# Kernel tuning notes

Hardware: AMD Instinct MI355X
Metric: run time of the kernel (lower is better)

The kernel has to match this reference:

```python
import jax, jax.numpy as jnp
import numpy as np
import math

C = 16
K = 16
M = 64
DEPTH = 4          # int(sqrt(K)) tree depth
D = C * 9          # input feature dim, 9 dims per codebook subspace
N = 1024 * 128     # rows
N_NODES = K - 1    # 15 internal nodes of a depth-4 binary tree


def _selection_matrix(C):
    # node i at tree level l reads the per-codebook hashed feature at depth index l
    S = np.zeros((C * N_NODES, C * DEPTH), np.float32)
    for c in range(C):
        for i in range(N_NODES):
            level = 0 if i == 0 else (1 if i < 3 else (2 if i < 7 else 3))
            S[c * N_NODES + i, c * DEPTH + level] = 1.0
    return S


def _bit_matrix(C, K):
    # row (c,k): +/-1 on the 4 tree nodes along code k's root-to-leaf path;
    # matching code scores DEPTH, every other code scores <= DEPTH-2
    B = np.zeros((C * K, C * N_NODES), np.float32)
    for c in range(C):
        for k in range(K):
            prefix = 0
            for l in range(DEPTH):
                bit = (k >> (DEPTH - 1 - l)) & 1
                node = (2 ** l - 1) + prefix
                B[c * K + k, c * N_NODES + node] = 1.0 if bit else -1.0
                prefix = prefix * 2 + bit
    return B


def setup_inputs() -> dict:
    key = jax.random.key(0)
    k1, k2, k3, k4 = jax.random.split(key, 4)
    I = jax.random.normal(k1, (N, D), jnp.float32) - 0.5
    A = jax.random.normal(k2, (C, D // C, DEPTH), jnp.float32)   # soft hashing projections
    T = jax.random.normal(k3, (C * N_NODES,), jnp.float32)       # node thresholds
    bound = math.sqrt(1.0 / (C * K))  # kaiming_uniform with a=sqrt(5), fan_in=C*K
    L = jax.random.uniform(k4, (M, C, K), jnp.float32, -bound, bound)  # lookup tables
    S = jnp.asarray(_selection_matrix(C))
    B = jnp.asarray(_bit_matrix(C, K))
    return {"I": I, "A": A, "T": T, "L": L, "S": S, "B": B}


def reference(I, A, T, L, S, B):
    n = I.shape[0]
    # per-codebook soft hash: (n, C, D//C) x (C, D//C, DEPTH) -> (n, C*DEPTH)
    h = jnp.einsum('ncd,cdp->ncp', I.reshape(n, C, D // C), A).reshape(n, C * DEPTH)
    # thresholded tree decisions with straight-through sign
    b = h @ S.T - T                                   # (n, C*15)
    t = jnp.tanh(b)
    s = jax.lax.stop_gradient(jnp.sign(b) - t) + t    # fwd: sign, bwd: tanh'
    # bit-matrix decode of path agreements -> per-code scores
    scores = (s @ B.T).reshape(n, C, K)               # (n, C, K), max DEPTH at true code
    onehot = jax.nn.one_hot(jnp.argmax(scores, axis=2), K, dtype=I.dtype)
    E = jax.lax.stop_gradient(onehot - scores) + scores  # STE one-hot encoding
    # LUT gather-accumulate: out[n,m] = sum_c L[m,c,code(n,c)]
    return jnp.einsum('nck,mck->nm', E, L)
```

## Files before the change

kernel.cpp:

```cpp
#include <hip/hip_runtime.h>
#include <hip/hip_fp16.h>


#define NROWS (1024 * 128)

__global__ __launch_bounds__(256, 4) void halut_fwd(
    const float* __restrict__ I,
    const float* __restrict__ A,
    const float* __restrict__ T,
    const float* __restrict__ L,
    float* __restrict__ out)
{
    __shared__ uint32_t sBuf[8192];
    __shared__ double   sA[576];
    __shared__ double   sT[240];

    const int tid = threadIdx.x;

    {
        uint2* lut2 = (uint2*)sBuf;
        #pragma unroll
        for (int q = 0; q < 16; ++q) {
            const float a = L[(4 * q + 0) * 256 + tid];
            const float b = L[(4 * q + 1) * 256 + tid];
            const float c = L[(4 * q + 2) * 256 + tid];
            const float d = L[(4 * q + 3) * 256 + tid];
            uint2 u;
            u.x = ((uint32_t)__half_as_ushort(__float2half_rn(b)) << 16)
                |  (uint32_t)__half_as_ushort(__float2half_rn(a));
            u.y = ((uint32_t)__half_as_ushort(__float2half_rn(d)) << 16)
                |  (uint32_t)__half_as_ushort(__float2half_rn(c));
            lut2[q * 256 + tid] = u;
        }
    }
    for (int i = tid; i < 576; i += 256) sA[i] = (double)A[i];
    if (tid < 240) sT[tid] = (double)T[tid];
    __syncthreads();

    const int lr  = tid >> 1;
    const int mh  = tid & 1;
    const int row = blockIdx.x * 128 + lr;
    const float* rp = I + (size_t)row * 144 + mh * 72;

    float4 buf[18];
    {
        const float4* rv = (const float4*)rp;
        #pragma unroll
        for (int i = 0; i < 18; ++i) buf[i] = rv[i];
    }
    const float* bf = (const float*)buf;

    uint32_t mycodes = 0;
    #pragma unroll
    for (int cl = 0; cl < 8; ++cl) {
        const int c = mh * 8 + cl;
        double h0 = 0.0, h1 = 0.0, h2 = 0.0, h3 = 0.0;
        #pragma unroll
        for (int d = 0; d < 9; ++d) {
            const double  x  = (double)bf[cl * 9 + d];
            const double* ap = &sA[(c * 9 + d) * 4];
            h0 = fma(x, ap[0], h0);
            h1 = fma(x, ap[1], h1);
            h2 = fma(x, ap[2], h2);
            h3 = fma(x, ap[3], h3);
        }
        const double* tp = &sT[c * 15];
        int p;
        p =         (h0 > tp[0]);
        p = 2 * p + (h1 > tp[1 + p]);
        p = 2 * p + (h2 > tp[3 + p]);
        p = 2 * p + (h3 > tp[7 + p]);
        mycodes |= (uint32_t)p << (4 * cl);
    }
    const uint32_t other = __shfl_xor(mycodes, 1);
    const uint32_t lo = mh ? other : mycodes;
    const uint32_t hi = mh ? mycodes : other;

    __half2 acc2[16];
    const __half2 zero = __floats2half2_rn(0.f, 0.f);
    #pragma unroll
    for (int k = 0; k < 16; ++k) acc2[k] = zero;

    const uint2* lut2 = (const uint2*)sBuf;
    #pragma unroll 4
    for (int c = 0; c < 16; ++c) {
        const int p   = (int)(((c < 8 ? lo : hi) >> (4 * (c & 7))) & 15u);
        const int col = (c << 4) + p;
        #pragma unroll
        for (int i = 0; i < 8; ++i) {
            const uint2 w = lut2[((mh * 8 + i) << 8) + col];
            const __half2 w0 = *(const __half2*)&w.x;
            const __half2 w1 = *(const __half2*)&w.y;
            acc2[2 * i]     = __hadd2(acc2[2 * i],     w0);
            acc2[2 * i + 1] = __hadd2(acc2[2 * i + 1], w1);
        }
    }

    __syncthreads();
    float* sO = (float*)sBuf;
    #pragma unroll
    for (int k2 = 0; k2 < 8; ++k2) {
        const int ch = mh * 8 + k2;
        const float4 v = make_float4(__low2float(acc2[2 * k2]),
                                     __high2float(acc2[2 * k2]),
                                     __low2float(acc2[2 * k2 + 1]),
                                     __high2float(acc2[2 * k2 + 1]));
        *(float4*)&sO[(lr << 6) + ((ch ^ (lr & 15)) << 2)] = v;
    }
    __syncthreads();

    float4* op = (float4*)(out + (size_t)blockIdx.x * (128 * 64));
    #pragma unroll
    for (int j = 0; j < 8; ++j) {
        const int F  = tid + (j << 8);
        const int r2 = F >> 4;
        const int m2 = F & 15;
        op[F] = *(const float4*)&sO[(r2 << 6) + ((m2 ^ (r2 & 15)) << 2)];
    }
}

extern "C" void kernel_launch(void* const* d_in, const int* in_sizes, int n_in,
                              void* d_out, int out_size, void* d_ws, size_t ws_size,
                              hipStream_t stream) {
    const float* I = (const float*)d_in[0];
    const float* A = (const float*)d_in[1];
    const float* T = (const float*)d_in[2];
    const float* L = (const float*)d_in[3];
    float* outp = (float*)d_out;

    const int nblocks = NROWS / 128;
    halut_fwd<<<nblocks, 256, 0, stream>>>(I, A, T, L, outp);
}
```

Measured before the change: 31.39 us.

## Split fused kernel into code-computation and LUT-gather kernels via workspace

Splits the single fused kernel into two launches: one computes the per-row 4-bit codes from the input projections and writes them to a workspace buffer, and the other loads the LUT into shared memory and does the gather-accumulate and output store. The code kernel also loads the input row in two halves of 9 float4 instead of 18, which lowers register pressure. The intent is to shrink each kernel's register and LDS footprint so occupancy rises and memory streaming overlaps better. In exchange it adds a second launch, a global round trip for the codes, and each gather block still rebuilds the LUT in shared memory.

```diff
diff --git a/kernel.cpp b/kernel.cpp
--- a/kernel.cpp
+++ b/kernel.cpp
@@ -4,16 +4,66 @@
 
 #define NROWS (1024 * 128)
 
-__global__ __launch_bounds__(256, 4) void halut_fwd(
+__global__ __launch_bounds__(256, 4) void halut_codes(
     const float* __restrict__ I,
     const float* __restrict__ A,
     const float* __restrict__ T,
+    uint32_t* __restrict__ codes)
+{
+    __shared__ double sA[576];
+    __shared__ double sT[240];
+
+    const int tid = threadIdx.x;
+    for (int i = tid; i < 576; i += 256) sA[i] = (double)A[i];
+    if (tid < 240) sT[tid] = (double)T[tid];
+    __syncthreads();
+
+    const int lr  = tid >> 1;
+    const int mh  = tid & 1;
+    const int row = blockIdx.x * 128 + lr;
+    const float* rp = I + (size_t)row * 144 + mh * 72;
+
+    uint32_t mycodes = 0;
+    #pragma unroll
+    for (int g = 0; g < 2; ++g) {
+        float4 buf[9];
+        const float4* rv = (const float4*)(rp + g * 36);
+        #pragma unroll
+        for (int i = 0; i < 9; ++i) buf[i] = rv[i];
+        const float* bf = (const float*)buf;
+
+        #pragma unroll
+        for (int cc = 0; cc < 4; ++cc) {
+            const int cl = g * 4 + cc;
+            const int c  = mh * 8 + cl;
+            double h0 = 0.0, h1 = 0.0, h2 = 0.0, h3 = 0.0;
+            #pragma unroll
+            for (int d = 0; d < 9; ++d) {
+                const double  x  = (double)bf[cc * 9 + d];
+                const double* ap = &sA[(c * 9 + d) * 4];
+                h0 = fma(x, ap[0], h0);
+                h1 = fma(x, ap[1], h1);
+                h2 = fma(x, ap[2], h2);
+                h3 = fma(x, ap[3], h3);
+            }
+            const double* tp = &sT[c * 15];
+            int p;
+            p =         (h0 > tp[0]);
+            p = 2 * p + (h1 > tp[1 + p]);
+            p = 2 * p + (h2 > tp[3 + p]);
+            p = 2 * p + (h3 > tp[7 + p]);
+            mycodes |= (uint32_t)p << (4 * cl);
+        }
+    }
+    codes[blockIdx.x * 256 + tid] = mycodes;
+}
+
+__global__ __launch_bounds__(256, 4) void halut_gather(
     const float* __restrict__ L,
+    const uint32_t* __restrict__ codes,
     float* __restrict__ out)
 {
     __shared__ uint32_t sBuf[8192];
-    __shared__ double   sA[576];
-    __shared__ double   sT[240];
 
     const int tid = threadIdx.x;
 
@@ -33,48 +83,15 @@
             lut2[q * 256 + tid] = u;
         }
     }
-    for (int i = tid; i < 576; i += 256) sA[i] = (double)A[i];
-    if (tid < 240) sT[tid] = (double)T[tid];
     __syncthreads();
 
     const int lr  = tid >> 1;
     const int mh  = tid & 1;
     const int row = blockIdx.x * 128 + lr;
-    const float* rp = I + (size_t)row * 144 + mh * 72;
 
-    float4 buf[18];
-    {
-        const float4* rv = (const float4*)rp;
-        #pragma unroll
-        for (int i = 0; i < 18; ++i) buf[i] = rv[i];
-    }
-    const float* bf = (const float*)buf;
-
-    uint32_t mycodes = 0;
-    #pragma unroll
-    for (int cl = 0; cl < 8; ++cl) {
-        const int c = mh * 8 + cl;
-        double h0 = 0.0, h1 = 0.0, h2 = 0.0, h3 = 0.0;
-        #pragma unroll
-        for (int d = 0; d < 9; ++d) {
-            const double  x  = (double)bf[cl * 9 + d];
-            const double* ap = &sA[(c * 9 + d) * 4];
-            h0 = fma(x, ap[0], h0);
-            h1 = fma(x, ap[1], h1);
-            h2 = fma(x, ap[2], h2);
-            h3 = fma(x, ap[3], h3);
-        }
-        const double* tp = &sT[c * 15];
-        int p;
-        p =         (h0 > tp[0]);
-        p = 2 * p + (h1 > tp[1 + p]);
-        p = 2 * p + (h2 > tp[3 + p]);
-        p = 2 * p + (h3 > tp[7 + p]);
-        mycodes |= (uint32_t)p << (4 * cl);
-    }
-    const uint32_t other = __shfl_xor(mycodes, 1);
-    const uint32_t lo = mh ? other : mycodes;
-    const uint32_t hi = mh ? mycodes : other;
+    const uint2 cw = ((const uint2*)codes)[row];
+    const uint32_t lo = cw.x;
+    const uint32_t hi = cw.y;
 
     __half2 acc2[16];
     const __half2 zero = __floats2half2_rn(0.f, 0.f);
@@ -127,7 +144,9 @@
     const float* T = (const float*)d_in[2];
     const float* L = (const float*)d_in[3];
     float* outp = (float*)d_out;
+    uint32_t* codes = (uint32_t*)d_ws;
 
     const int nblocks = NROWS / 128;
-    halut_fwd<<<nblocks, 256, 0, stream>>>(I, A, T, L, outp);
+    halut_codes <<<nblocks, 256, 0, stream>>>(I, A, T, codes);
+    halut_gather<<<nblocks, 256, 0, stream>>>(L, codes, outp);
 }
```

Measured after the change: 55.84 us. +77.9%, slower.
